# Kernel tuning notes

Hardware: AMD Instinct MI355X
Metric: run time of the kernel (lower is better)

The kernel has to match this reference:

```python
import jax, jax.numpy as jnp
import numpy as np

B, LSEQ, LQ = 16, 1024, 256
N_CTX, BIN = 8, 256
D, H, DEPTH = 1024, 16, 6
DFF = 4096
NEG = -1e9


def _ln(x, s, b, eps=1e-5):
    m = jnp.mean(x, axis=-1, keepdims=True)
    v = jnp.var(x, axis=-1, keepdims=True)
    return (x - m) * jax.lax.rsqrt(v + eps) * s + b


def setup_inputs() -> dict:
    key = jax.random.key(0)
    ks = jax.random.split(key, 16)
    s = 0.02
    return {
        "latents": jax.random.normal(ks[0], (B, LSEQ, D), jnp.float32),
        "in_time_idx": jax.random.randint(ks[1], (B, LSEQ), 0, BIN),
        "in_space_idx": jax.random.randint(ks[2], (B, LSEQ), 0, 32),
        "in_mask": jnp.ones((B, N_CTX + LSEQ), dtype=bool),
        "query_idx": jax.random.randint(ks[3], (B, LQ), 0, 2),
        "query_time_idx": jnp.sort(jax.random.randint(ks[4], (B, LQ), 0, BIN), axis=1),
        "query_space_idx": jax.random.randint(ks[5], (B, LQ), 0, 32),
        "query_mask": jnp.ones((B, LQ), dtype=bool),
        "ctx_emb": jax.random.normal(ks[6], (B, N_CTX, D), jnp.float32),
        "query_emb_w": s * jax.random.normal(ks[7], (2, D), jnp.float32),
        "time_emb_w": s * jax.random.normal(ks[8], (BIN, D), jnp.float32),
        "qkv_w": s * jax.random.normal(ks[9], (DEPTH, 3 * D, D), jnp.float32),
        "qkv_b": jnp.zeros((DEPTH, 3 * D), jnp.float32),
        "out_w": s * jax.random.normal(ks[10], (DEPTH, D, D), jnp.float32),
        "out_b": jnp.zeros((DEPTH, D), jnp.float32),
        "ln1_s": jnp.ones((DEPTH, D), jnp.float32),
        "ln1_b": jnp.zeros((DEPTH, D), jnp.float32),
        "ln2_s": jnp.ones((DEPTH, D), jnp.float32),
        "ln2_b": jnp.zeros((DEPTH, D), jnp.float32),
        "w1": s * jax.random.normal(ks[11], (DEPTH, DFF, D), jnp.float32),
        "b1": jnp.zeros((DEPTH, DFF), jnp.float32),
        "w2": s * jax.random.normal(ks[12], (DEPTH, D, DFF), jnp.float32),
        "b2": jnp.zeros((DEPTH, D), jnp.float32),
    }


def reference(latents, in_time_idx, in_space_idx, in_mask, query_idx,
              query_time_idx, query_space_idx, query_mask, ctx_emb,
              query_emb_w, time_emb_w, qkv_w, qkv_b, out_w, out_b,
              ln1_s, ln1_b, ln2_s, ln2_b, w1, b1, w2, b2):
    # ---- _pool: scatter-reduce mean of latents into (B, BIN, D) ----
    seq_mask = in_mask[:, N_CTX:]                               # (B, LSEQ)
    idx = jnp.where(seq_mask, in_time_idx, BIN)                 # masked -> trash bin
    oneh = jax.nn.one_hot(idx, BIN + 1, dtype=latents.dtype)    # (B, LSEQ, BIN+1)
    sums = jnp.einsum('bls,bld->bsd', oneh, latents)            # (B, BIN+1, D)
    cnts = jnp.sum(oneh, axis=1)                                # (B, BIN+1)
    pooled = (sums / jnp.maximum(cnts, 1.0)[:, :, None])[:, :BIN]

    pooled_time = jnp.broadcast_to(jnp.arange(BIN), (B, BIN))
    dec_time_idx = jnp.concatenate([pooled_time, query_time_idx], axis=1)  # (B, BIN+LQ)

    x = jnp.concatenate([pooled, query_emb_w[query_idx]], axis=1)
    x = x + time_emb_w[dec_time_idx]
    x = jnp.concatenate([jax.lax.stop_gradient(ctx_emb), x], axis=1)  # (B, L, D)
    L = N_CTX + BIN + LQ

    # ---- per-sample causal + context attention mask (True = blocked) ----
    blocked = jnp.zeros((B, L, L), dtype=bool)
    blocked = blocked.at[:, :N_CTX, N_CTX:].set(True)
    blocked = blocked.at[:, N_CTX:, N_CTX:].set(
        dec_time_idx[:, :, None] < dec_time_idx[:, None, :])
    pad = jnp.concatenate([jnp.zeros((B, N_CTX + BIN), bool), ~query_mask], axis=1)
    blocked = blocked | pad[:, None, :]
    bias = jnp.where(blocked, NEG, 0.0).astype(x.dtype)[:, None]  # (B,1,L,L)

    dh = D // H
    scale = 1.0 / np.sqrt(dh).astype(np.float32)

    def layer(h, p):
        qw, qb, ow, ob, l1s, l1b, l2s, l2b, fw1, fb1, fw2, fb2 = p
        # pre-norm self-attention
        y = _ln(h, l1s, l1b)
        qkv = y @ qw.T + qb
        q, k, v = jnp.split(qkv, 3, axis=-1)
        q = q.reshape(B, L, H, dh)
        k = k.reshape(B, L, H, dh)
        v = v.reshape(B, L, H, dh)
        scores = jnp.einsum('bihd,bjhd->bhij', q, k) * scale + bias
        a = jax.nn.softmax(scores, axis=-1)
        o = jnp.einsum('bhij,bjhd->bihd', a, v).reshape(B, L, D)
        h = h + o @ ow.T + ob
        # pre-norm FFN (exact GELU, as torch default)
        y = _ln(h, l2s, l2b)
        h = h + jax.nn.gelu(y @ fw1.T + fb1, approximate=False) @ fw2.T + fb2
        return h, None

    x, _ = jax.lax.scan(
        layer, x,
        (qkv_w, qkv_b, out_w, out_b, ln1_s, ln1_b, ln2_s, ln2_b, w1, b1, w2, b2))
    return x[:, N_CTX:]  # (B, BIN+LQ, D)
```

## Files before the change

kernel.cpp:

```cpp
#include <hip/hip_runtime.h>

#define B_    16
#define NCTX  8
#define BIN_  256
#define LQ_   256
#define L_    520
#define LSEQ  1024
#define D_    1024
#define H_    16
#define DH    64
#define DFF_  4096
#define DEPTH 6
#define MROWS (B_ * L_)
#define GY    65

using bf16x8 = __attribute__((ext_vector_type(8))) __bf16;
using bf16x4 = __attribute__((ext_vector_type(4))) __bf16;
using f32x4  = __attribute__((ext_vector_type(4))) float;

#define DEV __device__ __forceinline__

DEV int swz(int r, int c) { return (r << 6) + (((c ^ r) & 7) << 3); }

#define GLDS16(g, l)                                                         \
  __builtin_amdgcn_global_load_lds(                                          \
      (__attribute__((address_space(1))) void*)(g),                          \
      (__attribute__((address_space(3))) void*)(l), 16, 0, 0)


__global__ void te_k(const int* __restrict__ qtime, const int* __restrict__ tIdx,
                     int* __restrict__ Te, int* __restrict__ TeMinK,
                     int* __restrict__ TeMaxQ, int* __restrict__ cnts) {
  int b = blockIdx.x, pos = threadIdx.x;
  __shared__ int smin[9], smax[9], hc[256];
  if (pos < 9) { smin[pos] = 0x7fffffff; smax[pos] = (int)0x80000000; }
  if (pos < 256) hc[pos] = 0;
  __syncthreads();
  int v;
  if (pos < NCTX) v = (int)0x80000000;
  else if (pos < NCTX + BIN_) v = pos - NCTX;
  else if (pos < L_) v = qtime[b * LQ_ + (pos - NCTX - BIN_)];
  else v = 0x7fffffff;
  Te[b * 576 + pos] = v;
  int vq = (pos < L_) ? v : (int)0x80000000;
  atomicMin(&smin[pos >> 6], v);
  atomicMax(&smax[pos >> 6], vq);
  for (int i = pos; i < LSEQ; i += 576) atomicAdd(&hc[tIdx[b * LSEQ + i]], 1);
  __syncthreads();
  if (pos < 9) { TeMinK[b * 9 + pos] = smin[pos]; TeMaxQ[b * 9 + pos] = smax[pos]; }
  if (pos < 256) cnts[b * 256 + pos] = hc[pos];
}

__global__ __launch_bounds__(256) void pool_k(const float* __restrict__ latents,
                                              const int* __restrict__ tIdx,
                                              const int* __restrict__ cnts,
                                              const float* __restrict__ temb,
                                              float* __restrict__ h) {
  const int cg = blockIdx.x, b = blockIdx.y, tid = threadIdx.x;
  __shared__ float acc[256][33];
  __shared__ int sIdx[LSEQ];
  float* af = &acc[0][0];
  for (int i = tid; i < 256 * 33; i += 256) af[i] = 0.f;
#pragma unroll
  for (int j = 0; j < 4; ++j) sIdx[tid + 256 * j] = tIdx[b * LSEQ + tid + 256 * j];
  __syncthreads();
  const int col = tid & 31, rp = tid >> 5;
  const float* Lb = latents + (size_t)b * LSEQ * D_ + cg * 32 + col;
  for (int r = rp; r < LSEQ; r += 8)
    atomicAdd(&acc[sIdx[r]][col], Lb[(size_t)r * D_]);
  __syncthreads();
  for (int s = rp; s < 256; s += 8) {
    int c = cnts[b * 256 + s];
    float inv = 1.f / (float)(c > 0 ? c : 1);
    h[((size_t)b * L_ + NCTX + s) * D_ + cg * 32 + col] =
        acc[s][col] * inv + temb[(size_t)s * D_ + cg * 32 + col];
  }
}

__global__ void qrows_k(const float* __restrict__ ctx,
                        const float* __restrict__ qemb,
                        const float* __restrict__ temb,
                        const int* __restrict__ qidx,
                        const int* __restrict__ qtime, float* __restrict__ h) {
  int r = blockIdx.x, b = blockIdx.y, tid = threadIdx.x;
  if (r < NCTX) {
    float4 v = ((const float4*)(ctx + ((size_t)b * NCTX + r) * D_))[tid];
    ((float4*)(h + ((size_t)b * L_ + r) * D_))[tid] = v;
  } else {
    int q = r - NCTX;
    int qi = qidx[b * LQ_ + q];
    int qt = qtime[b * LQ_ + q];
    float4 e = ((const float4*)(qemb + (size_t)qi * D_))[tid];
    float4 t = ((const float4*)(temb + (size_t)qt * D_))[tid];
    float4 o; o.x = e.x + t.x; o.y = e.y + t.y; o.z = e.z + t.z; o.w = e.w + t.w;
    ((float4*)(h + ((size_t)b * L_ + NCTX + BIN_ + q) * D_))[tid] = o;
  }
}

__global__ void cvt4_k(const float* __restrict__ s0, const float* __restrict__ s1,
                       const float* __restrict__ s2, const float* __restrict__ s3,
                       __bf16* __restrict__ dst) {
  int i = blockIdx.x * 256 + threadIdx.x;
  const float* s; int off;
  if (i < 786432)       { s = s0; off = i; }
  else if (i < 1048576) { s = s1; off = i - 786432; }
  else if (i < 2097152) { s = s2; off = i - 1048576; }
  else                  { s = s3; off = i - 2097152; }
  float4 v = ((const float4*)s)[off];
  bf16x4 o;
  o[0] = (__bf16)v.x; o[1] = (__bf16)v.y; o[2] = (__bf16)v.z; o[3] = (__bf16)v.w;
  ((bf16x4*)dst)[i] = o;
}

__global__ __launch_bounds__(256) void ln_k(const float* __restrict__ h,
                                            const float* __restrict__ s,
                                            const float* __restrict__ bb,
                                            __bf16* __restrict__ y) {
  int row = blockIdx.x, tid = threadIdx.x;
  int lane = tid & 63, wave = tid >> 6;
  float4 v = ((const float4*)(h + (size_t)row * D_))[tid];
  float sum = v.x + v.y + v.z + v.w;
  float sq  = v.x * v.x + v.y * v.y + v.z * v.z + v.w * v.w;
#pragma unroll
  for (int m = 32; m; m >>= 1) { sum += __shfl_xor(sum, m); sq += __shfl_xor(sq, m); }
  __shared__ float red[8];
  if (lane == 0) { red[wave] = sum; red[4 + wave] = sq; }
  __syncthreads();
  sum = red[0] + red[1] + red[2] + red[3];
  sq  = red[4] + red[5] + red[6] + red[7];
  float mean = sum * (1.f / D_);
  float var  = sq * (1.f / D_) - mean * mean;
  float rstd = rsqrtf(var + 1e-5f);
  float4 sv = ((const float4*)s)[tid];
  float4 bv = ((const float4*)bb)[tid];
  bf16x4 o;
  o[0] = (__bf16)((v.x - mean) * rstd * sv.x + bv.x);
  o[1] = (__bf16)((v.y - mean) * rstd * sv.y + bv.y);
  o[2] = (__bf16)((v.z - mean) * rstd * sv.z + bv.z);
  o[3] = (__bf16)((v.w - mean) * rstd * sv.w + bv.w);
  *(bf16x4*)(y + (size_t)row * D_ + tid * 4) = o;
}

template <int EPI>
__global__ __launch_bounds__(256) void gemm_k(const __bf16* __restrict__ A,
                                              const __bf16* __restrict__ Bw,
                                              const float* __restrict__ bias,
                                              __bf16* __restrict__ outB,
                                              float* __restrict__ outF,
                                              int N, int K, int gx) {
  __shared__ __bf16 sA[128 * 64];
  __shared__ __bf16 sB[128 * 64];
  const int tid = threadIdx.x;
  const int lane = tid & 63, wave = tid >> 6;
  const int lr = lane & 15, lq = lane >> 4;
  const int wr = wave >> 1, wc = wave & 1;

  const int nwg = gridDim.x;
  int hid = blockIdx.x;
  int lid = (hid & 7) * (nwg >> 3) + (hid >> 3);
  int per_band = gx << 3;
  int band = lid / per_band;
  int rem = lid - band * per_band;
  int rows = min(8, GY - (band << 3));
  int by = (band << 3) + rem % rows;
  int bx = rem / rows;
  const size_t bm = (size_t)by * 128;
  const size_t bn = (size_t)bx * 128;

  f32x4 acc[4][4] = {};

  int stage_r[4], stage_src[4];
#pragma unroll
  for (int j = 0; j < 4; ++j) {
    int q = (wave * 4 + j) * 64 + lane;
    int r = q >> 3, c = q & 7;
    stage_r[j] = r;
    stage_src[j] = ((c ^ r) & 7) << 3;
  }
  const __bf16* Ab = A + bm * (size_t)K;
  const __bf16* Bb = Bw + bn * (size_t)K;
  const int nk = K >> 6;
  for (int kt = 0; kt < nk; ++kt) {
    const __bf16* Ak = Ab + kt * 64;
    const __bf16* Bk = Bb + kt * 64;
#pragma unroll
    for (int j = 0; j < 4; ++j) {
      int r = stage_r[j];
      GLDS16(Ak + (size_t)r * K + stage_src[j], sA + (wave * 4 + j) * 512);
      GLDS16(Bk + (size_t)r * K + stage_src[j], sB + (wave * 4 + j) * 512);
    }
    __syncthreads();
#pragma unroll
    for (int kk = 0; kk < 2; ++kk) {
      bf16x8 af[4], bfm[4];
#pragma unroll
      for (int im = 0; im < 4; ++im)
        af[im] = *(const bf16x8*)(sA + swz(wr * 64 + im * 16 + lr, kk * 4 + lq));
#pragma unroll
      for (int in = 0; in < 4; ++in)
        bfm[in] = *(const bf16x8*)(sB + swz(wc * 64 + in * 16 + lr, kk * 4 + lq));
#pragma unroll
      for (int im = 0; im < 4; ++im)
#pragma unroll
        for (int in = 0; in < 4; ++in)
          acc[im][in] = __builtin_amdgcn_mfma_f32_16x16x32_bf16(af[im], bfm[in], acc[im][in], 0, 0, 0);
    }
    __syncthreads();
  }
  const int r0 = (int)bm + wr * 64 + lq * 4;
  const int c0 = (int)bn + wc * 64 + lr;
#pragma unroll
  for (int in = 0; in < 4; ++in) {
    int cg = c0 + in * 16;
    float bl = bias[cg];
#pragma unroll
    for (int im = 0; im < 4; ++im) {
      f32x4 v = acc[im][in];
#pragma unroll
      for (int i = 0; i < 4; ++i) {
        int rg = r0 + im * 16 + i;
        float val = v[i] + bl;
        if (EPI == 0) {
          outB[(size_t)rg * N + cg] = (__bf16)val;
        } else if (EPI == 1) {
          outF[(size_t)rg * N + cg] += val;
        } else {
          float g = 0.5f * val * (1.0f + erff(val * 0.70710678118f));
          outB[(size_t)rg * N + cg] = (__bf16)g;
        }
      }
    }
  }
}

__global__ __launch_bounds__(512) void attn_k(const __bf16* __restrict__ qkv,
                                              const int* __restrict__ Te,
                                              const int* __restrict__ TeMinK,
                                              const int* __restrict__ TeMaxQ,
                                              __bf16* __restrict__ o) {
  const int qt = blockIdx.x, hh = blockIdx.y, b = blockIdx.z;
  const int tid = threadIdx.x;
  const int lane = tid & 63, wave = tid >> 6;
  const int lr = lane & 15, lq = lane >> 4;
  __shared__ __bf16 sQ[128 * 64], sK[64 * 64], sV[64 * 64];
  __shared__ __bf16 sP[8][16 * 64];
  __shared__ int sTq[128], sTk[64];

  if (tid < 128) {
    int rg = qt * 128 + tid;
    sTq[tid] = (rg < 576) ? Te[b * 576 + rg] : 0x7fffffff;
  }
  int maxQ = TeMaxQ[b * 9 + qt * 2];
  if (qt * 2 + 1 < 9) maxQ = max(maxQ, TeMaxQ[b * 9 + qt * 2 + 1]);

  const __bf16* base = qkv + (size_t)b * L_ * (3 * D_) + hh * DH;
#pragma unroll
  for (int j = 0; j < 2; ++j) {
    int q = tid + j * 512;
    int r = q >> 3, c = q & 7;
    int rg = qt * 128 + r;
    bf16x8 v = {};
    if (rg < L_) v = *(const bf16x8*)(base + (size_t)rg * (3 * D_) + c * 8);
    *(bf16x8*)(sQ + swz(r, c)) = v;
  }

  float m_run[4], l_run[4];
#pragma unroll
  for (int i = 0; i < 4; ++i) { m_run[i] = -1e30f; l_run[i] = 0.f; }
  f32x4 oacc[4] = {};
  const float scale = 0.125f;

  for (int kt = 0; kt < 9; ++kt) {
    if (TeMinK[b * 9 + kt] > maxQ) continue;
    __syncthreads();
    if (tid < 64) sTk[tid] = Te[b * 576 + kt * 64 + tid];
    {
      int r = tid >> 3, c = tid & 7;
      int rg = kt * 64 + r;
      bf16x8 kv = {}, vv = {};
      if (rg < L_) {
        kv = *(const bf16x8*)(base + D_ + (size_t)rg * (3 * D_) + c * 8);
        vv = *(const bf16x8*)(base + 2 * D_ + (size_t)rg * (3 * D_) + c * 8);
      }
      *(bf16x8*)(sK + swz(r, c)) = kv;
      *(bf16x8*)(sV + r * 64 + c * 8) = vv;
    }
    __syncthreads();

    f32x4 sacc[4] = {};
    __builtin_amdgcn_s_setprio(1);
#pragma unroll
    for (int kk = 0; kk < 2; ++kk) {
      bf16x8 aq = *(const bf16x8*)(sQ + swz(wave * 16 + lr, kk * 4 + lq));
#pragma unroll
      for (int cn = 0; cn < 4; ++cn) {
        bf16x8 bk = *(const bf16x8*)(sK + swz(cn * 16 + lr, kk * 4 + lq));
        sacc[cn] = __builtin_amdgcn_mfma_f32_16x16x32_bf16(aq, bk, sacc[cn], 0, 0, 0);
      }
    }
    __builtin_amdgcn_s_setprio(0);
    float sval[4][4], mt[4];
#pragma unroll
    for (int i = 0; i < 4; ++i) mt[i] = -1e30f;
#pragma unroll
    for (int cn = 0; cn < 4; ++cn) {
      int tk = sTk[cn * 16 + lr];
#pragma unroll
      for (int i = 0; i < 4; ++i) {
        int tq = sTq[wave * 16 + lq * 4 + i];
        float sv = sacc[cn][i] * scale + ((tq < tk) ? -1e9f : 0.f);
        sval[cn][i] = sv;
        mt[i] = fmaxf(mt[i], sv);
      }
    }
#pragma unroll
    for (int i = 0; i < 4; ++i) {
#pragma unroll
      for (int m = 1; m < 16; m <<= 1) mt[i] = fmaxf(mt[i], __shfl_xor(mt[i], m));
    }
    float fsc[4], lt[4];
    __bf16* sPw = sP[wave];
#pragma unroll
    for (int i = 0; i < 4; ++i) {
      float mnew = fmaxf(m_run[i], mt[i]);
      fsc[i] = __expf(m_run[i] - mnew);
      m_run[i] = mnew;
      lt[i] = 0.f;
    }
#pragma unroll
    for (int cn = 0; cn < 4; ++cn) {
#pragma unroll
      for (int i = 0; i < 4; ++i) {
        float p = __expf(sval[cn][i] - m_run[i]);
        lt[i] += p;
        int rp = lq * 4 + i;
        int kvx = cn * 16 + lr;
        sPw[(rp << 6) + ((((kvx >> 3) ^ rp) & 7) << 3) + (kvx & 7)] = (__bf16)p;
      }
    }
#pragma unroll
    for (int i = 0; i < 4; ++i) {
#pragma unroll
      for (int m = 1; m < 16; m <<= 1) lt[i] += __shfl_xor(lt[i], m);
      l_run[i] = l_run[i] * fsc[i] + lt[i];
    }
#pragma unroll
    for (int dn = 0; dn < 4; ++dn)
#pragma unroll
      for (int i = 0; i < 4; ++i) oacc[dn][i] *= fsc[i];

    __builtin_amdgcn_s_setprio(1);
#pragma unroll
    for (int kk = 0; kk < 2; ++kk) {
      bf16x8 ap = *(const bf16x8*)(sPw + swz(lr, kk * 4 + lq));
#pragma unroll
      for (int dn = 0; dn < 4; ++dn) {
        bf16x8 bv;
#pragma unroll
        for (int i2 = 0; i2 < 8; ++i2)
          bv[i2] = sV[(kk * 32 + lq * 8 + i2) * 64 + dn * 16 + lr];
        oacc[dn] = __builtin_amdgcn_mfma_f32_16x16x32_bf16(ap, bv, oacc[dn], 0, 0, 0);
      }
    }
    __builtin_amdgcn_s_setprio(0);
  }
#pragma unroll
  for (int dn = 0; dn < 4; ++dn) {
#pragma unroll
    for (int i = 0; i < 4; ++i) {
      int rg = qt * 128 + wave * 16 + lq * 4 + i;
      if (rg < L_) {
        float val = oacc[dn][i] / l_run[i];
        o[((size_t)b * L_ + rg) * D_ + hh * DH + dn * 16 + lr] = (__bf16)val;
      }
    }
  }
}

__global__ void out_k(const float* __restrict__ h, float* __restrict__ out) {
  int idx = blockIdx.x * 256 + threadIdx.x;
  int c4 = idx & 255;
  int r = (idx >> 8) & 511;
  int b = idx >> 17;
  ((float4*)out)[idx] = ((const float4*)h)[((size_t)b * L_ + NCTX + r) * 256 + c4];
}

extern "C" void kernel_launch(void* const* d_in, const int* in_sizes, int n_in,
                              void* d_out, int out_size, void* d_ws, size_t ws_size,
                              hipStream_t stream) {
  const float* latents      = (const float*)d_in[0];
  const int*   in_time_idx  = (const int*)d_in[1];
  const int*   query_idx    = (const int*)d_in[4];
  const int*   query_time   = (const int*)d_in[5];
  const float* ctx_emb      = (const float*)d_in[8];
  const float* query_emb_w  = (const float*)d_in[9];
  const float* time_emb_w   = (const float*)d_in[10];
  const float* qkv_w        = (const float*)d_in[11];
  const float* qkv_b        = (const float*)d_in[12];
  const float* out_w        = (const float*)d_in[13];
  const float* out_b        = (const float*)d_in[14];
  const float* ln1_s        = (const float*)d_in[15];
  const float* ln1_b        = (const float*)d_in[16];
  const float* ln2_s        = (const float*)d_in[17];
  const float* ln2_b        = (const float*)d_in[18];
  const float* w1           = (const float*)d_in[19];
  const float* b1           = (const float*)d_in[20];
  const float* w2           = (const float*)d_in[21];
  const float* b2           = (const float*)d_in[22];

  size_t off = 0;
  auto alloc = [&](size_t n) { char* p = (char*)d_ws + off; off += (n + 255) & ~(size_t)255; return (void*)p; };
  float*  h    = (float*)alloc((size_t)MROWS * D_ * 4);
  __bf16* y    = (__bf16*)alloc((size_t)MROWS * D_ * 2);
  __bf16* qkvb = (__bf16*)alloc((size_t)MROWS * 3 * D_ * 2);
  __bf16* mid  = (__bf16*)alloc((size_t)MROWS * DFF_ * 2);
  __bf16* wsl  = (__bf16*)alloc((size_t)12582912 * 2);
  int*    Te   = (int*)alloc((size_t)B_ * 576 * 4);
  int*    TeMn = (int*)alloc((size_t)B_ * 9 * 4);
  int*    TeMx = (int*)alloc((size_t)B_ * 9 * 4);
  int*    Cnt  = (int*)alloc((size_t)B_ * 256 * 4);
  (void)ws_size; (void)in_sizes; (void)n_in; (void)out_size;
  __bf16* wq  = wsl;
  __bf16* wo  = wsl + 3145728;
  __bf16* w1b = wsl + 4194304;
  __bf16* w2b = wsl + 8388608;

  te_k<<<B_, 576, 0, stream>>>(query_time, in_time_idx, Te, TeMn, TeMx, Cnt);
  pool_k<<<dim3(32, B_), 256, 0, stream>>>(latents, in_time_idx, Cnt, time_emb_w, h);
  qrows_k<<<dim3(NCTX + LQ_, B_), 256, 0, stream>>>(ctx_emb, query_emb_w, time_emb_w,
                                                    query_idx, query_time, h);
  for (int l = 0; l < DEPTH; ++l) {
    cvt4_k<<<12288, 256, 0, stream>>>(qkv_w + (size_t)l * 3145728, out_w + (size_t)l * 1048576,
                                      w1 + (size_t)l * 4194304, w2 + (size_t)l * 4194304, wsl);

    ln_k<<<MROWS, 256, 0, stream>>>(h, ln1_s + l * D_, ln1_b + l * D_, y);
    gemm_k<0><<<24 * GY, 256, 0, stream>>>(
        y, wq, qkv_b + (size_t)l * 3 * D_, qkvb, nullptr, 3 * D_, D_, 24);
    attn_k<<<dim3(5, H_, B_), 512, 0, stream>>>(qkvb, Te, TeMn, TeMx, y);
    gemm_k<1><<<8 * GY, 256, 0, stream>>>(
        y, wo, out_b + (size_t)l * D_, nullptr, h, D_, D_, 8);
    ln_k<<<MROWS, 256, 0, stream>>>(h, ln2_s + l * D_, ln2_b + l * D_, y);
    gemm_k<2><<<32 * GY, 256, 0, stream>>>(
        y, w1b, b1 + (size_t)l * DFF_, mid, nullptr, DFF_, D_, 32);
    gemm_k<1><<<8 * GY, 256, 0, stream>>>(
        mid, w2b, b2 + (size_t)l * D_, nullptr, h, D_, DFF_, 8);
  }
  out_k<<<(B_ * 512 * 256) / 256, 256, 0, stream>>>(h, (float*)d_out);
}
```

Baseline: 3.055 ms.

## Retile attention to 64-row query tiles, use wave-per-row LayerNorm, fuse final output copy

Attention now runs 64-query tiles with 256 threads over a 9x16x16 grid instead of 128-query tiles with 512 threads. This gives more blocks and finer causal-style tile skipping, but each K/V tile is reloaded by more blocks. LayerNorm handles one row per wave with four rows per block, which removes the shared-memory reduction and the block barrier. The last layer's FFN-down GEMM writes the residual sum straight into the output tensor, so the separate slicing copy kernel is gone.

```diff
diff --git a/kernel.cpp b/kernel.cpp
--- a/kernel.cpp
+++ b/kernel.cpp
@@ -116,29 +116,33 @@
                                             const float* __restrict__ s,
                                             const float* __restrict__ bb,
                                             __bf16* __restrict__ y) {
-  int row = blockIdx.x, tid = threadIdx.x;
-  int lane = tid & 63, wave = tid >> 6;
-  float4 v = ((const float4*)(h + (size_t)row * D_))[tid];
-  float sum = v.x + v.y + v.z + v.w;
-  float sq  = v.x * v.x + v.y * v.y + v.z * v.z + v.w * v.w;
+  const int lane = threadIdx.x & 63, wave = threadIdx.x >> 6;
+  const int row = blockIdx.x * 4 + wave;
+  const float4* hr = (const float4*)(h + (size_t)row * D_);
+  float4 v[4];
+  float sum = 0.f, sq = 0.f;
+#pragma unroll
+  for (int j = 0; j < 4; ++j) {
+    v[j] = hr[lane + 64 * j];
+    sum += v[j].x + v[j].y + v[j].z + v[j].w;
+    sq += v[j].x * v[j].x + v[j].y * v[j].y + v[j].z * v[j].z + v[j].w * v[j].w;
+  }
 #pragma unroll
   for (int m = 32; m; m >>= 1) { sum += __shfl_xor(sum, m); sq += __shfl_xor(sq, m); }
-  __shared__ float red[8];
-  if (lane == 0) { red[wave] = sum; red[4 + wave] = sq; }
-  __syncthreads();
-  sum = red[0] + red[1] + red[2] + red[3];
-  sq  = red[4] + red[5] + red[6] + red[7];
   float mean = sum * (1.f / D_);
   float var  = sq * (1.f / D_) - mean * mean;
   float rstd = rsqrtf(var + 1e-5f);
-  float4 sv = ((const float4*)s)[tid];
-  float4 bv = ((const float4*)bb)[tid];
-  bf16x4 o;
-  o[0] = (__bf16)((v.x - mean) * rstd * sv.x + bv.x);
-  o[1] = (__bf16)((v.y - mean) * rstd * sv.y + bv.y);
-  o[2] = (__bf16)((v.z - mean) * rstd * sv.z + bv.z);
-  o[3] = (__bf16)((v.w - mean) * rstd * sv.w + bv.w);
-  *(bf16x4*)(y + (size_t)row * D_ + tid * 4) = o;
+#pragma unroll
+  for (int j = 0; j < 4; ++j) {
+    float4 sv = ((const float4*)s)[lane + 64 * j];
+    float4 bv = ((const float4*)bb)[lane + 64 * j];
+    bf16x4 o;
+    o[0] = (__bf16)((v[j].x - mean) * rstd * sv.x + bv.x);
+    o[1] = (__bf16)((v[j].y - mean) * rstd * sv.y + bv.y);
+    o[2] = (__bf16)((v[j].z - mean) * rstd * sv.z + bv.z);
+    o[3] = (__bf16)((v[j].w - mean) * rstd * sv.w + bv.w);
+    *(bf16x4*)(y + (size_t)row * D_ + (lane + 64 * j) * 4) = o;
+  }
 }
 
 template <int EPI>
@@ -147,6 +151,7 @@
                                               const float* __restrict__ bias,
                                               __bf16* __restrict__ outB,
                                               float* __restrict__ outF,
+                                              float* __restrict__ outD,
                                               int N, int K, int gx) {
   __shared__ __bf16 sA[128 * 64];
   __shared__ __bf16 sB[128 * 64];
@@ -224,16 +229,22 @@
           outB[(size_t)rg * N + cg] = (__bf16)val;
         } else if (EPI == 1) {
           outF[(size_t)rg * N + cg] += val;
-        } else {
+        } else if (EPI == 2) {
           float g = 0.5f * val * (1.0f + erff(val * 0.70710678118f));
           outB[(size_t)rg * N + cg] = (__bf16)g;
+        } else {
+          float hv = outF[(size_t)rg * N + cg] + val;
+          int bb2 = rg / 520;
+          int rr = rg - bb2 * 520;
+          if (rr >= NCTX)
+            outD[((size_t)bb2 * 512 + (rr - NCTX)) * 1024 + cg] = hv;
         }
       }
     }
   }
 }
 
-__global__ __launch_bounds__(512) void attn_k(const __bf16* __restrict__ qkv,
+__global__ __launch_bounds__(256) void attn_k(const __bf16* __restrict__ qkv,
                                               const int* __restrict__ Te,
                                               const int* __restrict__ TeMinK,
                                               const int* __restrict__ TeMaxQ,
@@ -242,23 +253,19 @@
   const int tid = threadIdx.x;
   const int lane = tid & 63, wave = tid >> 6;
   const int lr = lane & 15, lq = lane >> 4;
-  __shared__ __bf16 sQ[128 * 64], sK[64 * 64], sV[64 * 64];
-  __shared__ __bf16 sP[8][16 * 64];
-  __shared__ int sTq[128], sTk[64];
-
-  if (tid < 128) {
-    int rg = qt * 128 + tid;
-    sTq[tid] = (rg < 576) ? Te[b * 576 + rg] : 0x7fffffff;
-  }
-  int maxQ = TeMaxQ[b * 9 + qt * 2];
-  if (qt * 2 + 1 < 9) maxQ = max(maxQ, TeMaxQ[b * 9 + qt * 2 + 1]);
+  __shared__ __bf16 sQ[64 * 64], sK[64 * 64], sV[64 * 64];
+  __shared__ __bf16 sP[4][16 * 64];
+  __shared__ int sTq[64], sTk[64];
+
+  if (tid < 64) sTq[tid] = Te[b * 576 + qt * 64 + tid];
+  const int maxQ = TeMaxQ[b * 9 + qt];
 
   const __bf16* base = qkv + (size_t)b * L_ * (3 * D_) + hh * DH;
 #pragma unroll
   for (int j = 0; j < 2; ++j) {
-    int q = tid + j * 512;
+    int q = tid + j * 256;
     int r = q >> 3, c = q & 7;
-    int rg = qt * 128 + r;
+    int rg = qt * 64 + r;
     bf16x8 v = {};
     if (rg < L_) v = *(const bf16x8*)(base + (size_t)rg * (3 * D_) + c * 8);
     *(bf16x8*)(sQ + swz(r, c)) = v;
@@ -274,8 +281,10 @@
     if (TeMinK[b * 9 + kt] > maxQ) continue;
     __syncthreads();
     if (tid < 64) sTk[tid] = Te[b * 576 + kt * 64 + tid];
-    {
-      int r = tid >> 3, c = tid & 7;
+#pragma unroll
+    for (int j = 0; j < 2; ++j) {
+      int q = tid + j * 256;
+      int r = q >> 3, c = q & 7;
       int rg = kt * 64 + r;
       bf16x8 kv = {}, vv = {};
       if (rg < L_) {
@@ -368,21 +377,13 @@
   for (int dn = 0; dn < 4; ++dn) {
 #pragma unroll
     for (int i = 0; i < 4; ++i) {
-      int rg = qt * 128 + wave * 16 + lq * 4 + i;
+      int rg = qt * 64 + wave * 16 + lq * 4 + i;
       if (rg < L_) {
         float val = oacc[dn][i] / l_run[i];
         o[((size_t)b * L_ + rg) * D_ + hh * DH + dn * 16 + lr] = (__bf16)val;
       }
     }
   }
-}
-
-__global__ void out_k(const float* __restrict__ h, float* __restrict__ out) {
-  int idx = blockIdx.x * 256 + threadIdx.x;
-  int c4 = idx & 255;
-  int r = (idx >> 8) & 511;
-  int b = idx >> 17;
-  ((float4*)out)[idx] = ((const float4*)h)[((size_t)b * L_ + NCTX + r) * 256 + c4];
 }
 
 extern "C" void kernel_launch(void* const* d_in, const int* in_sizes, int n_in,
@@ -433,17 +434,21 @@
     cvt4_k<<<12288, 256, 0, stream>>>(qkv_w + (size_t)l * 3145728, out_w + (size_t)l * 1048576,
                                       w1 + (size_t)l * 4194304, w2 + (size_t)l * 4194304, wsl);
 
-    ln_k<<<MROWS, 256, 0, stream>>>(h, ln1_s + l * D_, ln1_b + l * D_, y);
+    ln_k<<<MROWS / 4, 256, 0, stream>>>(h, ln1_s + l * D_, ln1_b + l * D_, y);
     gemm_k<0><<<24 * GY, 256, 0, stream>>>(
-        y, wq, qkv_b + (size_t)l * 3 * D_, qkvb, nullptr, 3 * D_, D_, 24);
-    attn_k<<<dim3(5, H_, B_), 512, 0, stream>>>(qkvb, Te, TeMn, TeMx, y);
+        y, wq, qkv_b + (size_t)l * 3 * D_, qkvb, nullptr, nullptr, 3 * D_, D_, 24);
+    attn_k<<<dim3(9, H_, B_), 256, 0, stream>>>(qkvb, Te, TeMn, TeMx, y);
     gemm_k<1><<<8 * GY, 256, 0, stream>>>(
-        y, wo, out_b + (size_t)l * D_, nullptr, h, D_, D_, 8);
-    ln_k<<<MROWS, 256, 0, stream>>>(h, ln2_s + l * D_, ln2_b + l * D_, y);
+        y, wo, out_b + (size_t)l * D_, nullptr, h, nullptr, D_, D_, 8);
+    ln_k<<<MROWS / 4, 256, 0, stream>>>(h, ln2_s + l * D_, ln2_b + l * D_, y);
     gemm_k<2><<<32 * GY, 256, 0, stream>>>(
-        y, w1b, b1 + (size_t)l * DFF_, mid, nullptr, DFF_, D_, 32);
-    gemm_k<1><<<8 * GY, 256, 0, stream>>>(
-        mid, w2b, b2 + (size_t)l * D_, nullptr, h, D_, DFF_, 8);
-  }
-  out_k<<<(B_ * 512 * 256) / 256, 256, 0, stream>>>(h, (float*)d_out);
-}
+        y, w1b, b1 + (size_t)l * DFF_, mid, nullptr, nullptr, DFF_, D_, 32);
+    if (l < DEPTH - 1) {
+      gemm_k<1><<<8 * GY, 256, 0, stream>>>(
+          mid, w2b, b2 + (size_t)l * D_, nullptr, h, nullptr, D_, DFF_, 8);
+    } else {
+      gemm_k<3><<<8 * GY, 256, 0, stream>>>(
+          mid, w2b, b2 + (size_t)l * D_, nullptr, h, (float*)d_out, D_, DFF_, 8);
+    }
+  }
+}
```

Result: no change. 3.015 ms (-1.3%).
